# Kernel tuning notes

Hardware: AMD Instinct MI355X
Metric: run time of the kernel (lower is better)

The kernel has to match this reference:

```python
import jax, jax.numpy as jnp
import numpy as np

B, C, T = 1024, 64, 275
S = 10            # number of subjects
EMB = 184         # encoder embedding dim
PROJ = 1024       # projector dim
LN_EPS = 1e-5


def setup_inputs() -> dict:
    key = jax.random.key(0)
    ks = jax.random.split(key, 12)
    sc = lambda *shape: 1.0 / np.sqrt(shape[-1] if len(shape) > 1 else 1.0)
    return {
        "eeg": jax.random.normal(ks[0], (B, C, T), dtype=jnp.float32),
        "subject_ids": jax.random.randint(ks[1], (B,), 0, S, dtype=jnp.int64),
        # per-subject Linear(T, T): y = x @ W.T + b
        "subj_W": jax.random.normal(ks[2], (S, T, T), dtype=jnp.float32) / np.sqrt(T),
        "subj_b": jax.random.normal(ks[3], (S, T), dtype=jnp.float32) * 0.02,
        # encoder stub: flatten (C*T) -> Linear -> EMB
        "enc_W": jax.random.normal(ks[4], (C * T, EMB), dtype=jnp.float32) / np.sqrt(C * T),
        "enc_b": jnp.zeros((EMB,), dtype=jnp.float32),
        # projector: Linear(EMB, PROJ) -> ResidualAdd(GELU -> Linear(PROJ, PROJ)) -> LayerNorm
        "W1": jax.random.normal(ks[5], (EMB, PROJ), dtype=jnp.float32) / np.sqrt(EMB),
        "b1": jnp.zeros((PROJ,), dtype=jnp.float32),
        "W2": jax.random.normal(ks[6], (PROJ, PROJ), dtype=jnp.float32) / np.sqrt(PROJ),
        "b2": jnp.zeros((PROJ,), dtype=jnp.float32),
        "gamma": jnp.ones((PROJ,), dtype=jnp.float32),
        "beta": jnp.zeros((PROJ,), dtype=jnp.float32),
    }


def reference(eeg, subject_ids, subj_W, subj_b, enc_W, enc_b, W1, b1, W2, b2, gamma, beta):
    # --- subject-wise alignment: grouped gather -> linear -> scatter ---
    # Vectorized form of the per-subject loop: each row b uses weight subj_W[sid[b]].
    Wg = subj_W[subject_ids]              # [B, T, T]
    bg = subj_b[subject_ids]              # [B, T]
    # torch Linear: y = x @ W.T + b  ->  y[b,c,u] = sum_t eeg[b,c,t] * Wg[b,u,t]
    x = jnp.einsum("bct,but->bcu", eeg, Wg) + bg[:, None, :]   # [B, C, T]

    # --- encoder stub (SpatioTemporalCNN placeholder): flatten + linear ---
    h = x.reshape(x.shape[0], -1) @ enc_W + enc_b              # [B, EMB]

    # --- MLPProjector ---
    h = h @ W1 + b1                                            # [B, PROJ]
    r = jax.nn.gelu(h, approximate=False) @ W2 + b2            # dropout is identity at eval
    h = h + r
    # LayerNorm over last dim
    mu = jnp.mean(h, axis=-1, keepdims=True)
    var = jnp.mean(jnp.square(h - mu), axis=-1, keepdims=True)
    out = (h - mu) * jax.lax.rsqrt(var + LN_EPS) * gamma + beta
    return out
```

## Files before the change

kernel.cpp:

```cpp
#include <hip/hip_runtime.h>
#include <hip/hip_bf16.h>
#include <math.h>

#define B_N    1024
#define C_N    64
#define T_N    275
#define S_N    10
#define EMB_N  184
#define PROJ_N 1024
#define CT_N   (C_N * T_N)
#define TP     288
#define KP2    (C_N * TP)
#define EMBP   192
#define KZ2    16
#define KC2    (KP2 / KZ2)
#define KZ5    2
#define GMAX   264
#define ESTR   296

#define SEC_W   0
#define SEC_E   810
#define SEC_1   1002
#define SEC_2   1050
#define SEC_G   1306
#define SEC_N   1307

typedef unsigned short u16;
typedef __attribute__((ext_vector_type(8))) short short8;
typedef __attribute__((ext_vector_type(4))) short short4v;
typedef __attribute__((ext_vector_type(4))) float f32x4;

#define MFMA16(a,b,c) __builtin_amdgcn_mfma_f32_16x16x32_bf16(a, b, c, 0, 0, 0)

__device__ __forceinline__ u16 f2bf(float f) {
    __hip_bfloat16 h = __float2bfloat16(f);
    return *reinterpret_cast<u16*>(&h);
}
__device__ __forceinline__ float gelu_exact(float v) {
    return 0.5f * v * (1.0f + erff(v * 0.70710678118654752f));
}
__device__ __forceinline__ void gload16(const void* g, void* lds) {
    __builtin_amdgcn_global_load_lds(
        (const __attribute__((address_space(1))) void*)g,
        (__attribute__((address_space(3))) void*)lds, 16, 0, 0);
}

__global__ __launch_bounds__(256) void p_all(
    const int* __restrict__ sid, const float* __restrict__ W,
    const float* __restrict__ encW, const float* __restrict__ W1,
    const float* __restrict__ W2, const float* __restrict__ subj_b,
    u16* __restrict__ Wb, u16* __restrict__ eT, u16* __restrict__ w1t,
    u16* __restrict__ w2t, int* __restrict__ bsq, float* __restrict__ sbp)
{
    __shared__ char smem[16640];
    const int blk = blockIdx.x;
    const int tid = threadIdx.x;

    if (blk < SEC_E) {
        int idx4 = blk * 256 + tid;
        if (idx4 >= S_N * TP * TP / 4) return;
        int o = idx4 * 4;
        int row = o / TP, t = o - row * TP;
        int s = row / TP, u = row - s * TP;
        short4v pk;
        #pragma unroll
        for (int e = 0; e < 4; ++e) {
            float v = (u < T_N && t + e < T_N)
                ? W[((size_t)s * T_N + u) * T_N + t + e] : 0.f;
            pk[e] = (short)f2bf(v);
        }
        *reinterpret_cast<short4v*>(Wb + o) = pk;
        return;
    }
    if (blk < SEC_1) {
        float (*tile)[65] = (float(*)[65])smem;
        int local = blk - SEC_E;
        const int c = local / 3;
        const int n0 = (local % 3) * 64;
        for (int u0 = 0; u0 < TP; u0 += 64) {
            int wlen = (TP - u0 < 64) ? (TP - u0) : 64;
            __syncthreads();
            for (int l = tid; l < 4096; l += 256) {
                int i = l >> 6, j = l & 63;
                int u = u0 + i, n = n0 + j;
                float v = 0.f;
                if (u < T_N && n < EMB_N)
                    v = encW[((size_t)c * T_N + u) * EMB_N + n];
                tile[i][j] = v;
            }
            __syncthreads();
            for (int l = tid; l < 4096; l += 256) {
                int j = l >> 6, i = l & 63;
                if (i < wlen)
                    eT[(size_t)(n0 + j) * KP2 + (size_t)c * TP + u0 + i] =
                        f2bf(tile[i][j]);
            }
        }
        return;
    }
    if (blk < SEC_2) {
        float (*tile)[65] = (float(*)[65])smem;
        int local = blk - SEC_1;
        const int k0 = (local % 3) * 64, n0 = (local / 3) * 64;
        for (int l = tid; l < 4096; l += 256) {
            int i = l >> 6, j = l & 63;
            float v = (k0 + i < EMB_N) ? W1[(size_t)(k0 + i) * PROJ_N + n0 + j] : 0.f;
            tile[i][j] = v;
        }
        __syncthreads();
        for (int l = tid; l < 4096; l += 256) {
            int j = l >> 6, i = l & 63;
            w1t[(size_t)(n0 + j) * EMBP + k0 + i] = f2bf(tile[i][j]);
        }
        return;
    }
    if (blk < SEC_G) {
        float (*tile)[65] = (float(*)[65])smem;
        int local = blk - SEC_2;
        const int k0 = (local % 16) * 64, n0 = (local / 16) * 64;
        for (int l = tid; l < 4096; l += 256) {
            int i = l >> 6, j = l & 63;
            tile[i][j] = W2[(size_t)(k0 + i) * PROJ_N + n0 + j];
        }
        __syncthreads();
        for (int l = tid; l < 4096; l += 256) {
            int j = l >> 6, i = l & 63;
            w2t[(size_t)(n0 + j) * PROJ_N + k0 + i] = f2bf(tile[i][j]);
        }
        return;
    }
    {
        for (int i = tid; i < S_N * TP; i += 256) {
            int s = i / TP, u = i - s * TP;
            sbp[i] = (u < T_N) ? subj_b[s * T_N + u] : 0.f;
        }
        int* sgrp = (int*)smem;
        int* C    = (int*)(smem + 4096);
        int* tot  = (int*)(smem + 4096 + 640);
        for (int i = tid; i < 1024; i += 256) sgrp[i] = sid[i];
        for (int i = tid; i < 4 * GMAX; i += 256) bsq[i] = -1;
        __syncthreads();
        const int w4 = tid >> 6, lane = tid & 63;
        #pragma unroll
        for (int j = 0; j < 4; ++j) {
            int chunk = w4 * 4 + j;
            int sb = sgrp[chunk * 64 + lane];
            int myc = 0;
            for (int s = 0; s < S_N; ++s) {
                unsigned long long m = __ballot(sb == s);
                if (lane == s) myc = (int)__popcll(m);
            }
            if (lane < S_N) C[chunk * S_N + lane] = myc;
        }
        __syncthreads();
        if (tid < S_N) {
            int a = 0;
            for (int w2 = 0; w2 < 16; ++w2) a += C[w2 * S_N + tid];
            tot[tid] = a;
        }
        __syncthreads();
        #pragma unroll
        for (int rep = 0; rep < 4; ++rep) {
            int b = tid + rep * 256;
            int s = sgrp[b];
            int off = 0;
            for (int s2 = 0; s2 < S_N; ++s2)
                if (s2 < s) off += (tot[s2] + 3) & ~3;
            int chunk = b >> 6;
            int rank = 0;
            for (int w2 = 0; w2 < 16; ++w2)
                if (w2 < chunk) rank += C[w2 * S_N + s];
            for (int i = chunk * 64; i < b; ++i) rank += (sgrp[i] == s) ? 1 : 0;
            bsq[off + rank] = b;
        }
    }
}

__global__ __launch_bounds__(256) void k1v(
    const float* __restrict__ eeg, const int* __restrict__ sid,
    const u16* __restrict__ Wb, const float* __restrict__ sbp,
    const int* __restrict__ bsq, u16* __restrict__ xb)
{
    __shared__ __align__(16) u16 Es[64 * ESTR];
    __shared__ __align__(16) u16 Ws[2][TP * 32];
    const int g = blockIdx.x;
    const int b0 = bsq[g * 4];
    if (b0 < 0) return;
    const int p = blockIdx.y >> 1, ch = blockIdx.y & 1;
    const int s = sid[b0];
    const int tid = threadIdx.x;
    const int w = tid >> 6, lane = tid & 63;
    const int bi = w >> 1, uh = w & 1;
    const int lrow = lane & 15, lk = lane >> 4;
    const int b = bsq[g * 4 + p * 2 + bi];
    const u16* Wr = Wb + (size_t)s * TP * TP;

    #define K1_WSTAGE(st, ks)                                                  \
        for (int l = tid; l < TP * 4; l += 256) {                              \
            int u_ = l >> 2, q_ = l & 3;                                       \
            gload16(Wr + (size_t)u_ * TP + (ks) * 32 + ((q_ ^ ((u_ >> 1) & 3)) << 3), \
                    &Ws[st][l * 8]);                                           \
        }

    K1_WSTAGE(0, 0);
    #pragma unroll
    for (int reg = 0; reg < 2; ++reg) {
        int bstage = bsq[g * 4 + p * 2 + reg]; if (bstage < 0) bstage = b0;
        const float4* src4 = reinterpret_cast<const float4*>(
            eeg + (size_t)bstage * CT_N + ch * 32 * T_N);
        for (int l = tid; l < (32 * T_N) / 4; l += 256) {
            float4 v = src4[l];
            float vv[4] = { v.x, v.y, v.z, v.w };
            int o = l * 4;
            int r = o / T_N, c0 = o - r * T_N;
            #pragma unroll
            for (int e = 0; e < 4; ++e) {
                int r2 = r, c2 = c0 + e;
                if (c2 >= T_N) { r2++; c2 -= T_N; }
                Es[(reg * 32 + r2) * ESTR + c2] = f2bf(vv[e]);
            }
        }
    }
    for (int l = tid; l < 64 * (TP - T_N); l += 256) {
        int r = l / (TP - T_N), c = T_N + (l - r * (TP - T_N));
        Es[r * ESTR + c] = 0;
    }
    __syncthreads();

    f32x4 acc[9][2] = {};
    for (int ks = 0; ks < 9; ++ks) {
        const int st = ks & 1;
        if (ks < 8) K1_WSTAGE(st ^ 1, ks + 1);
        short8 ef[2];
        #pragma unroll
        for (int cf = 0; cf < 2; ++cf)
            ef[cf] = *reinterpret_cast<const short8*>(
                &Es[(bi * 32 + cf * 16 + lrow) * ESTR + ks * 32 + lk * 8]);
        #pragma unroll
        for (int uf = 0; uf < 9; ++uf) {
            int u = uh * 144 + uf * 16 + lrow;
            int chunk = u * 4 + (lk ^ ((u >> 1) & 3));
            short8 av = *reinterpret_cast<const short8*>(&Ws[st][chunk * 8]);
            acc[uf][0] = MFMA16(av, ef[0], acc[uf][0]);
            acc[uf][1] = MFMA16(av, ef[1], acc[uf][1]);
        }
        __syncthreads();
    }

    if (b < 0) return;
    u16* xrow = xb + (size_t)b * KP2 + (size_t)(ch * 32) * TP;
    #pragma unroll
    for (int uf = 0; uf < 9; ++uf) {
        int ub = uh * 144 + uf * 16 + 4 * lk;
        float4 b4 = *reinterpret_cast<const float4*>(sbp + s * TP + ub);
        float bias[4] = { b4.x, b4.y, b4.z, b4.w };
        #pragma unroll
        for (int cf = 0; cf < 2; ++cf) {
            int c = cf * 16 + lrow;
            short4v pk;
            #pragma unroll
            for (int r = 0; r < 4; ++r)
                pk[r] = (ub + r < T_N) ? (short)f2bf(acc[uf][cf][r] + bias[r])
                                       : (short)0;
            *reinterpret_cast<short4v*>(xrow + (size_t)c * TP + ub) = pk;
        }
    }
    #undef K1_WSTAGE
}

__global__ __launch_bounds__(256) void k2_mfma(
    const u16* __restrict__ xb, const u16* __restrict__ eT,
    float* __restrict__ part)
{
    __shared__ __align__(16) u16 Ab[2][64 * 64];
    const int m0 = blockIdx.x * 64;
    const int kz = blockIdx.y;
    const int kbase = kz * KC2;
    const int tid = threadIdx.x;
    const int w = tid >> 6, lane = tid & 63;
    const int lrow = lane & 15, lk = lane >> 4;

    #define K2_STAGE(st, step)                                                 \
        _Pragma("unroll")                                                      \
        for (int p = 0; p < 2; ++p) {                                          \
            int l = tid + p * 256;                                             \
            int r_ = l >> 3, q_ = l & 7;                                       \
            gload16(xb + (size_t)(m0 + r_) * KP2 + kbase + (step) * 64 +       \
                        ((q_ ^ (r_ & 7)) << 3),                                \
                    &Ab[st][l * 8]);                                           \
        }
    #define K2_BLOAD(step, dst)                                                \
        _Pragma("unroll")                                                      \
        for (int ct = 0; ct < 3; ++ct)                                         \
            _Pragma("unroll")                                                  \
            for (int ki = 0; ki < 2; ++ki)                                     \
                dst[ct][ki] = *reinterpret_cast<const short8*>(                \
                    eT + (size_t)(48 * w + 16 * ct + lrow) * KP2 + kbase +     \
                    (step) * 64 + ki * 32 + 8 * lk);

    f32x4 acc[4][3] = {};
    short8 bf[3][2], bn[3][2];

    K2_STAGE(0, 0);
    K2_BLOAD(0, bf);
    __syncthreads();

    for (int step = 0; step < 18; ++step) {
        const int st = step & 1;
        if (step < 17) {
            K2_STAGE(st ^ 1, step + 1);
            K2_BLOAD(step + 1, bn);
        }
        #pragma unroll
        for (int ki = 0; ki < 2; ++ki)
            #pragma unroll
            for (int rt = 0; rt < 4; ++rt) {
                int m = 16 * rt + lrow;
                int chunk = m * 8 + ((4 * ki + lk) ^ (m & 7));
                short8 af = *reinterpret_cast<const short8*>(&Ab[st][chunk * 8]);
                #pragma unroll
                for (int ct = 0; ct < 3; ++ct)
                    acc[rt][ct] = MFMA16(af, bf[ct][ki], acc[rt][ct]);
            }
        __syncthreads();
        #pragma unroll
        for (int ct = 0; ct < 3; ++ct)
            #pragma unroll
            for (int ki = 0; ki < 2; ++ki) bf[ct][ki] = bn[ct][ki];
    }

    #pragma unroll
    for (int rt = 0; rt < 4; ++rt)
        #pragma unroll
        for (int ct = 0; ct < 3; ++ct) {
            int n = 48 * w + 16 * ct + lrow;
            #pragma unroll
            for (int r = 0; r < 4; ++r) {
                int m = m0 + 16 * rt + 4 * lk + r;
                part[((size_t)kz * B_N + m) * EMBP + n] = acc[rt][ct][r];
            }
        }
    #undef K2_STAGE
    #undef K2_BLOAD
}

__global__ __launch_bounds__(256) void k3_reduce(
    const float* __restrict__ part, const float* __restrict__ enc_b,
    u16* __restrict__ hb)
{
    int idx = blockIdx.x * 256 + threadIdx.x;
    if (idx >= B_N * EMBP) return;
    int n = idx % EMBP;
    float s = 0.f;
    if (n < EMB_N) {
        s = enc_b[n];
        #pragma unroll
        for (int z = 0; z < KZ2; ++z)
            s += part[(size_t)z * B_N * EMBP + idx];
    }
    hb[idx] = f2bf(s);
}

__global__ __launch_bounds__(256) void k4_mfma(
    const u16* __restrict__ hb, const u16* __restrict__ w1t,
    const float* __restrict__ b1, float* __restrict__ h1, u16* __restrict__ g)
{
    __shared__ __align__(16) u16 Ab[64 * EMBP];
    __shared__ __align__(16) u16 Bb[64 * EMBP];
    const int m0 = blockIdx.x * 64, n0 = blockIdx.y * 64;
    const int tid = threadIdx.x;
    const int w = tid >> 6, lane = tid & 63;
    const int wr = w >> 1, wc = w & 1;
    const int lrow = lane & 15, lk = lane >> 4;

    #pragma unroll
    for (int i = 0; i < 6; ++i) {
        int L = tid + i * 256;
        int row = L / 24, qp = L % 24;
        int ql = qp ^ (row & 7);
        gload16(hb  + (size_t)(m0 + row) * EMBP + ql * 8, &Ab[(size_t)L * 8]);
        gload16(w1t + (size_t)(n0 + row) * EMBP + ql * 8, &Bb[(size_t)L * 8]);
    }
    __syncthreads();

    f32x4 acc[2][2] = {};
    #pragma unroll
    for (int ks = 0; ks < 6; ++ks) {
        #pragma unroll
        for (int rt = 0; rt < 2; ++rt) {
            int c = 32 * wr + 16 * rt + lrow;
            short8 af = *reinterpret_cast<const short8*>(
                &Ab[c * EMBP + (((4 * ks + lk) ^ (c & 7)) * 8)]);
            #pragma unroll
            for (int ct = 0; ct < 2; ++ct) {
                int nl = 32 * wc + 16 * ct + lrow;
                short8 bfv = *reinterpret_cast<const short8*>(
                    &Bb[nl * EMBP + (((4 * ks + lk) ^ (nl & 7)) * 8)]);
                acc[rt][ct] = MFMA16(af, bfv, acc[rt][ct]);
            }
        }
    }
    #pragma unroll
    for (int rt = 0; rt < 2; ++rt)
        #pragma unroll
        for (int ct = 0; ct < 2; ++ct) {
            int n = n0 + 32 * wc + 16 * ct + lrow;
            #pragma unroll
            for (int r = 0; r < 4; ++r) {
                int m = m0 + 32 * wr + 16 * rt + 4 * lk + r;
                float v = acc[rt][ct][r] + b1[n];
                size_t o = (size_t)m * PROJ_N + n;
                h1[o] = v;
                g[o] = f2bf(gelu_exact(v));
            }
        }
}

__global__ __launch_bounds__(256) void k5_mfma(
    const u16* __restrict__ g, const u16* __restrict__ w2t,
    float* __restrict__ part2)
{
    __shared__ __align__(16) u16 Ab[2][64 * 64];
    __shared__ __align__(16) u16 Bb[2][64 * 64];
    const int m0 = blockIdx.x * 64, n0 = blockIdx.y * 64;
    const int kz = blockIdx.z;
    const int kbase = kz * (PROJ_N / KZ5);
    const int tid = threadIdx.x;
    const int w = tid >> 6, lane = tid & 63;
    const int wr = w >> 1, wc = w & 1;
    const int lrow = lane & 15, lk = lane >> 4;

    const int r0 = tid >> 3, q0 = tid & 7;
    const int r1 = (tid + 256) >> 3;
    const u16* a0 = g + (size_t)(m0 + r0) * PROJ_N + (q0 ^ (r0 & 7)) * 8;
    const u16* a1 = g + (size_t)(m0 + r1) * PROJ_N + (q0 ^ (r1 & 7)) * 8;
    const u16* b0 = w2t + (size_t)(n0 + r0) * PROJ_N + (q0 ^ (r0 & 7)) * 8;
    const u16* b1p = w2t + (size_t)(n0 + r1) * PROJ_N + (q0 ^ (r1 & 7)) * 8;

    f32x4 acc[2][2] = {};
    int buf = 0;
    gload16(a0 + kbase, &Ab[0][(size_t)(w * 64) * 8]);
    gload16(a1 + kbase, &Ab[0][(size_t)(w * 64 + 256) * 8]);
    gload16(b0 + kbase, &Bb[0][(size_t)(w * 64) * 8]);
    gload16(b1p + kbase, &Bb[0][(size_t)(w * 64 + 256) * 8]);
    __syncthreads();

    for (int step = 0; step < 8; ++step) {
        if (step < 7) {
            int k0 = kbase + (step + 1) * 64;
            gload16(a0 + k0, &Ab[buf ^ 1][(size_t)(w * 64) * 8]);
            gload16(a1 + k0, &Ab[buf ^ 1][(size_t)(w * 64 + 256) * 8]);
            gload16(b0 + k0, &Bb[buf ^ 1][(size_t)(w * 64) * 8]);
            gload16(b1p + k0, &Bb[buf ^ 1][(size_t)(w * 64 + 256) * 8]);
        }
        #pragma unroll
        for (int ki = 0; ki < 2; ++ki) {
            #pragma unroll
            for (int rt = 0; rt < 2; ++rt) {
                int c = 32 * wr + 16 * rt + lrow;
                short8 af = *reinterpret_cast<const short8*>(
                    &Ab[buf][c * 64 + (((lk + 4 * ki) ^ (c & 7)) * 8)]);
                #pragma unroll
                for (int ct = 0; ct < 2; ++ct) {
                    int nl = 32 * wc + 16 * ct + lrow;
                    short8 bfv = *reinterpret_cast<const short8*>(
                        &Bb[buf][nl * 64 + (((lk + 4 * ki) ^ (nl & 7)) * 8)]);
                    acc[rt][ct] = MFMA16(af, bfv, acc[rt][ct]);
                }
            }
        }
        __syncthreads();
        buf ^= 1;
    }
    #pragma unroll
    for (int rt = 0; rt < 2; ++rt)
        #pragma unroll
        for (int ct = 0; ct < 2; ++ct) {
            int n = n0 + 32 * wc + 16 * ct + lrow;
            #pragma unroll
            for (int r = 0; r < 4; ++r) {
                int m = m0 + 32 * wr + 16 * rt + 4 * lk + r;
                part2[(size_t)kz * B_N * PROJ_N + (size_t)m * PROJ_N + n] = acc[rt][ct][r];
            }
        }
}

__global__ __launch_bounds__(256) void k5r_ln(
    const float* __restrict__ part2, const float* __restrict__ h1,
    const float* __restrict__ b2, const float* __restrict__ gamma,
    const float* __restrict__ beta, float* __restrict__ out)
{
    const int m = blockIdx.x;
    const int tid = threadIdx.x;
    const float4* h4 = reinterpret_cast<const float4*>(h1 + (size_t)m * PROJ_N);
    const float4* p0 = reinterpret_cast<const float4*>(part2 + (size_t)m * PROJ_N);
    const float4* p1 = reinterpret_cast<const float4*>(part2 + (size_t)(B_N + m) * PROJ_N);
    const float4* b4 = reinterpret_cast<const float4*>(b2);
    float4 va = h4[tid], vb = p0[tid], vc = p1[tid], vd = b4[tid];
    float v[4] = { va.x + vb.x + vc.x + vd.x, va.y + vb.y + vc.y + vd.y,
                   va.z + vb.z + vc.z + vd.z, va.w + vb.w + vc.w + vd.w };
    float s = 0.f, sq = 0.f;
    #pragma unroll
    for (int i = 0; i < 4; ++i) { s += v[i]; sq += v[i] * v[i]; }
    #pragma unroll
    for (int off = 32; off > 0; off >>= 1) {
        s  += __shfl_down(s, off);
        sq += __shfl_down(sq, off);
    }
    __shared__ float ss[4], ssq[4];
    int wid = tid >> 6, lane = tid & 63;
    if (lane == 0) { ss[wid] = s; ssq[wid] = sq; }
    __syncthreads();
    if (tid == 0) {
        float a = 0.f, bsum = 0.f;
        #pragma unroll
        for (int q = 0; q < 4; ++q) { a += ss[q]; bsum += ssq[q]; }
        ss[0] = a; ssq[0] = bsum;
    }
    __syncthreads();
    float mu  = ss[0] * (1.0f / PROJ_N);
    float var = ssq[0] * (1.0f / PROJ_N) - mu * mu;
    float rs  = rsqrtf(var + 1e-5f);
    const float4 g4 = reinterpret_cast<const float4*>(gamma)[tid];
    const float4 be4 = reinterpret_cast<const float4*>(beta)[tid];
    float gg[4] = { g4.x, g4.y, g4.z, g4.w };
    float bb[4] = { be4.x, be4.y, be4.z, be4.w };
    float4 o4;
    float* op = reinterpret_cast<float*>(&o4);
    #pragma unroll
    for (int i = 0; i < 4; ++i) op[i] = (v[i] - mu) * rs * gg[i] + bb[i];
    reinterpret_cast<float4*>(out + (size_t)m * PROJ_N)[tid] = o4;
}

extern "C" void kernel_launch(void* const* d_in, const int* in_sizes, int n_in,
                              void* d_out, int out_size, void* d_ws, size_t ws_size,
                              hipStream_t stream)
{
    const float* eeg    = (const float*)d_in[0];
    const int*   sid    = (const int*)  d_in[1];
    const float* subj_W = (const float*)d_in[2];
    const float* subj_b = (const float*)d_in[3];
    const float* enc_W  = (const float*)d_in[4];
    const float* enc_b  = (const float*)d_in[5];
    const float* W1     = (const float*)d_in[6];
    const float* b1     = (const float*)d_in[7];
    const float* W2     = (const float*)d_in[8];
    const float* b2     = (const float*)d_in[9];
    const float* gamma  = (const float*)d_in[10];
    const float* beta   = (const float*)d_in[11];
    float* out = (float*)d_out;

    char* w = (char*)d_ws;
    u16*   xb    = (u16*)(w);
    u16*   Wb    = (u16*)(w + 37748736);
    u16*   eT    = (u16*)(w + 39407616);
    u16*   w1t   = (u16*)(w + 46485504);
    u16*   w2t   = (u16*)(w + 46878720);
    u16*   hb    = (u16*)(w + 48975872);
    float* h1    = (float*)(w + 49369088);
    u16*   g     = (u16*)(w + 53563392);
    float* sbp   = (float*)(w + 55660544);
    int*   bsq   = (int*)(w + 55672064);
    float* part  = (float*)(w + 55676288);
    float* part2 = (float*)(w + 68259200);

    p_all<<<dim3(SEC_N), 256, 0, stream>>>(sid, subj_W, enc_W, W1, W2, subj_b,
                                           Wb, eT, w1t, w2t, bsq, sbp);
    k1v  <<<dim3(GMAX, 4), 256, 0, stream>>>(eeg, sid, Wb, sbp, bsq, xb);
    k2_mfma<<<dim3(16, KZ2), 256, 0, stream>>>(xb, eT, part);
    k3_reduce<<<dim3((B_N * EMBP + 255) / 256), 256, 0, stream>>>(part, enc_b, hb);
    k4_mfma<<<dim3(16, 16), 256, 0, stream>>>(hb, w1t, b1, h1, g);
    k5_mfma<<<dim3(16, 16, KZ5), 256, 0, stream>>>(g, w2t, part2);
    k5r_ln <<<dim3(B_N), 256, 0, stream>>>(part2, h1, b2, gamma, beta, out);
}
```

Baseline: 130.9 us.

## Pre-convert EEG to padded bf16 and stream it via async LDS loads in k1

The prep kernel gains 1024 extra blocks that convert each EEG sample to a zero-padded bf16 layout with row stride 288. The subject-linear kernel becomes a 512-thread block handling four samples per subject group. It double-buffers both the weight tile and the swizzled EEG tile through global_load_lds each k-step, replacing the up-front fp32 load, convert and LDS scatter. It also raises wave priority around the MFMA loop. The trade is an extra global write and read of the bf16 EEG copy, which reuses the partials scratch region, and larger blocks that may lower occupancy.

```diff
diff --git a/kernel.cpp b/kernel.cpp
--- a/kernel.cpp
+++ b/kernel.cpp
@@ -16,14 +16,14 @@
 #define KC2    (KP2 / KZ2)
 #define KZ5    2
 #define GMAX   264
-#define ESTR   296
-
-#define SEC_W   0
-#define SEC_E   810
-#define SEC_1   1002
-#define SEC_2   1050
-#define SEC_G   1306
-#define SEC_N   1307
+
+#define SEC_EEG 0
+#define SEC_W   1024
+#define SEC_E   1834
+#define SEC_1   2026
+#define SEC_2   2074
+#define SEC_G   2330
+#define SEC_N   2331
 
 typedef unsigned short u16;
 typedef __attribute__((ext_vector_type(8))) short short8;
@@ -46,18 +46,40 @@
 }
 
 __global__ __launch_bounds__(256) void p_all(
-    const int* __restrict__ sid, const float* __restrict__ W,
-    const float* __restrict__ encW, const float* __restrict__ W1,
-    const float* __restrict__ W2, const float* __restrict__ subj_b,
-    u16* __restrict__ Wb, u16* __restrict__ eT, u16* __restrict__ w1t,
-    u16* __restrict__ w2t, int* __restrict__ bsq, float* __restrict__ sbp)
+    const float* __restrict__ eeg, const int* __restrict__ sid,
+    const float* __restrict__ W, const float* __restrict__ encW,
+    const float* __restrict__ W1, const float* __restrict__ W2,
+    const float* __restrict__ subj_b,
+    u16* __restrict__ eegb, u16* __restrict__ Wb, u16* __restrict__ eT,
+    u16* __restrict__ w1t, u16* __restrict__ w2t, int* __restrict__ bsq,
+    float* __restrict__ sbp)
 {
     __shared__ char smem[16640];
     const int blk = blockIdx.x;
     const int tid = threadIdx.x;
 
+    if (blk < SEC_W) {
+        const int b = blk;
+        const float* src = eeg + (size_t)b * CT_N;
+        u16* dst = eegb + (size_t)b * (C_N * TP);
+        #pragma unroll
+        for (int p = 0; p < 9; ++p) {
+            int L = tid + p * 256;
+            int r = L / 36, q8 = L - r * 36;
+            int t0 = q8 * 8;
+            short8 pk;
+            #pragma unroll
+            for (int e = 0; e < 8; ++e) {
+                int t = t0 + e;
+                float v = (t < T_N) ? src[r * T_N + t] : 0.f;
+                pk[e] = (short)f2bf(v);
+            }
+            *reinterpret_cast<short8*>(dst + r * TP + t0) = pk;
+        }
+        return;
+    }
     if (blk < SEC_E) {
-        int idx4 = blk * 256 + tid;
+        int idx4 = (blk - SEC_W) * 256 + tid;
         if (idx4 >= S_N * TP * TP / 4) return;
         int o = idx4 * 4;
         int row = o / TP, t = o - row * TP;
@@ -176,66 +198,60 @@
     }
 }
 
-__global__ __launch_bounds__(256) void k1v(
-    const float* __restrict__ eeg, const int* __restrict__ sid,
+__global__ __launch_bounds__(512) void k1x(
+    const u16* __restrict__ eegb, const int* __restrict__ sid,
     const u16* __restrict__ Wb, const float* __restrict__ sbp,
     const int* __restrict__ bsq, u16* __restrict__ xb)
 {
-    __shared__ __align__(16) u16 Es[64 * ESTR];
     __shared__ __align__(16) u16 Ws[2][TP * 32];
+    __shared__ __align__(16) u16 Es[2][128 * 32];
     const int g = blockIdx.x;
     const int b0 = bsq[g * 4];
     if (b0 < 0) return;
-    const int p = blockIdx.y >> 1, ch = blockIdx.y & 1;
+    const int ch = blockIdx.y;
     const int s = sid[b0];
     const int tid = threadIdx.x;
     const int w = tid >> 6, lane = tid & 63;
     const int bi = w >> 1, uh = w & 1;
     const int lrow = lane & 15, lk = lane >> 4;
-    const int b = bsq[g * 4 + p * 2 + bi];
+    const int b = bsq[g * 4 + bi];
     const u16* Wr = Wb + (size_t)s * TP * TP;
 
+    const int ar = tid >> 2, aq = tid & 3;
+    int bsa = bsq[g * 4 + (ar >> 5)]; if (bsa < 0) bsa = b0;
+    const u16* asrc = eegb + (size_t)bsa * (C_N * TP)
+                    + (size_t)(ch * 32 + (ar & 31)) * TP
+                    + ((aq ^ ((ar >> 1) & 3)) << 3);
+
     #define K1_WSTAGE(st, ks)                                                  \
-        for (int l = tid; l < TP * 4; l += 256) {                              \
+        for (int l = tid; l < TP * 4; l += 512) {                              \
             int u_ = l >> 2, q_ = l & 3;                                       \
             gload16(Wr + (size_t)u_ * TP + (ks) * 32 + ((q_ ^ ((u_ >> 1) & 3)) << 3), \
                     &Ws[st][l * 8]);                                           \
         }
+    #define K1_ASTAGE(st, ks)                                                  \
+        gload16(asrc + (ks) * 32, &Es[st][tid * 8]);
+
+    f32x4 acc[9][2] = {};
 
     K1_WSTAGE(0, 0);
-    #pragma unroll
-    for (int reg = 0; reg < 2; ++reg) {
-        int bstage = bsq[g * 4 + p * 2 + reg]; if (bstage < 0) bstage = b0;
-        const float4* src4 = reinterpret_cast<const float4*>(
-            eeg + (size_t)bstage * CT_N + ch * 32 * T_N);
-        for (int l = tid; l < (32 * T_N) / 4; l += 256) {
-            float4 v = src4[l];
-            float vv[4] = { v.x, v.y, v.z, v.w };
-            int o = l * 4;
-            int r = o / T_N, c0 = o - r * T_N;
-            #pragma unroll
-            for (int e = 0; e < 4; ++e) {
-                int r2 = r, c2 = c0 + e;
-                if (c2 >= T_N) { r2++; c2 -= T_N; }
-                Es[(reg * 32 + r2) * ESTR + c2] = f2bf(vv[e]);
-            }
-        }
-    }
-    for (int l = tid; l < 64 * (TP - T_N); l += 256) {
-        int r = l / (TP - T_N), c = T_N + (l - r * (TP - T_N));
-        Es[r * ESTR + c] = 0;
-    }
+    K1_ASTAGE(0, 0);
     __syncthreads();
 
-    f32x4 acc[9][2] = {};
     for (int ks = 0; ks < 9; ++ks) {
         const int st = ks & 1;
-        if (ks < 8) K1_WSTAGE(st ^ 1, ks + 1);
+        if (ks < 8) {
+            K1_WSTAGE(st ^ 1, ks + 1);
+            K1_ASTAGE(st ^ 1, ks + 1);
+        }
         short8 ef[2];
         #pragma unroll
-        for (int cf = 0; cf < 2; ++cf)
+        for (int cf = 0; cf < 2; ++cf) {
+            int rr = bi * 32 + cf * 16 + lrow;
             ef[cf] = *reinterpret_cast<const short8*>(
-                &Es[(bi * 32 + cf * 16 + lrow) * ESTR + ks * 32 + lk * 8]);
+                &Es[st][(rr * 4 + (lk ^ ((rr >> 1) & 3))) * 8]);
+        }
+        __builtin_amdgcn_s_setprio(1);
         #pragma unroll
         for (int uf = 0; uf < 9; ++uf) {
             int u = uh * 144 + uf * 16 + lrow;
@@ -244,6 +260,7 @@
             acc[uf][0] = MFMA16(av, ef[0], acc[uf][0]);
             acc[uf][1] = MFMA16(av, ef[1], acc[uf][1]);
         }
+        __builtin_amdgcn_s_setprio(0);
         __syncthreads();
     }
 
@@ -266,6 +283,7 @@
         }
     }
     #undef K1_WSTAGE
+    #undef K1_ASTAGE
 }
 
 __global__ __launch_bounds__(256) void k2_mfma(
@@ -561,12 +579,15 @@
     u16*   g     = (u16*)(w + 53563392);
     float* sbp   = (float*)(w + 55660544);
     int*   bsq   = (int*)(w + 55672064);
-    float* part  = (float*)(w + 55676288);
-    float* part2 = (float*)(w + 68259200);
-
-    p_all<<<dim3(SEC_N), 256, 0, stream>>>(sid, subj_W, enc_W, W1, W2, subj_b,
-                                           Wb, eT, w1t, w2t, bsq, sbp);
-    k1v  <<<dim3(GMAX, 4), 256, 0, stream>>>(eeg, sid, Wb, sbp, bsq, xb);
+    char*  scr   = w + 55676288;
+    u16*   eegb  = (u16*)scr;
+    float* part  = (float*)scr;
+    float* part2 = (float*)(scr + 12582912);
+
+    p_all<<<dim3(SEC_N), 256, 0, stream>>>(eeg, sid, subj_W, enc_W, W1, W2,
+                                           subj_b, eegb, Wb, eT, w1t, w2t,
+                                           bsq, sbp);
+    k1x  <<<dim3(GMAX, 2), 512, 0, stream>>>(eegb, sid, Wb, sbp, bsq, xb);
     k2_mfma<<<dim3(16, KZ2), 256, 0, stream>>>(xb, eT, part);
     k3_reduce<<<dim3((B_N * EMBP + 255) / 256), 256, 0, stream>>>(part, enc_b, hb);
     k4_mfma<<<dim3(16, 16), 256, 0, stream>>>(hb, w1t, b1, h1, g);
```

Result: faster. 125.7 us (-4.0%).

## Restructure subject-alignment kernel into 512-thread blocks with pipelined async EEG loads

Applied to the files above, without the earlier changes.

Replaces k1v with k1y, which runs 8 waves per block and covers all four batch rows of a group. Each staged subject-weight tile is therefore reused across twice as many rows, halving the block count and the weight staging traffic. Instead of converting the whole EEG slab to bf16 in LDS before the loop, each k-step now async-loads a swizzled fp32 chunk with 4-byte global_load_lds, double-buffered alongside the weight tiles, and converts to bf16 when building fragments. It also raises wave priority around the MFMA block. The cost is more LDS instructions and conversions per step. The padded tail columns load column-0 data, which stays correct only because the padded weights are zero.

```diff
diff --git a/kernel.cpp b/kernel.cpp
--- a/kernel.cpp
+++ b/kernel.cpp
@@ -16,7 +16,6 @@
 #define KC2    (KP2 / KZ2)
 #define KZ5    2
 #define GMAX   264
-#define ESTR   296
 
 #define SEC_W   0
 #define SEC_E   810
@@ -43,6 +42,11 @@
     __builtin_amdgcn_global_load_lds(
         (const __attribute__((address_space(1))) void*)g,
         (__attribute__((address_space(3))) void*)lds, 16, 0, 0);
+}
+__device__ __forceinline__ void gload4(const void* g, void* lds) {
+    __builtin_amdgcn_global_load_lds(
+        (const __attribute__((address_space(1))) void*)g,
+        (__attribute__((address_space(3))) void*)lds, 4, 0, 0);
 }
 
 __global__ __launch_bounds__(256) void p_all(
@@ -176,66 +180,89 @@
     }
 }
 
-__global__ __launch_bounds__(256) void k1v(
+__global__ __launch_bounds__(512) void k1y(
     const float* __restrict__ eeg, const int* __restrict__ sid,
     const u16* __restrict__ Wb, const float* __restrict__ sbp,
     const int* __restrict__ bsq, u16* __restrict__ xb)
 {
-    __shared__ __align__(16) u16 Es[64 * ESTR];
-    __shared__ __align__(16) u16 Ws[2][TP * 32];
+    __shared__ __align__(16) u16   Ws[2][TP * 32];
+    __shared__ __align__(16) float Ea[2][128 * 32];
     const int g = blockIdx.x;
     const int b0 = bsq[g * 4];
     if (b0 < 0) return;
-    const int p = blockIdx.y >> 1, ch = blockIdx.y & 1;
+    const int ch = blockIdx.y;
     const int s = sid[b0];
     const int tid = threadIdx.x;
     const int w = tid >> 6, lane = tid & 63;
     const int bi = w >> 1, uh = w & 1;
     const int lrow = lane & 15, lk = lane >> 4;
-    const int b = bsq[g * 4 + p * 2 + bi];
+    const int b = bsq[g * 4 + bi];
     const u16* Wr = Wb + (size_t)s * TP * TP;
 
+    const int ep  = tid & 31;
+    const int re  = tid >> 5;
+    const int sel = (((ep >> 2) ^ (re & 7)) << 2) + (ep & 3);
+    const int sel8 = (256 + sel < T_N) ? (256 + sel) : 0;
+    const float* eb0; const float* eb1; const float* eb2; const float* eb3;
+    {
+        int b00 = bsq[g*4+0]; if (b00 < 0) b00 = b0;
+        int b01 = bsq[g*4+1]; if (b01 < 0) b01 = b0;
+        int b02 = bsq[g*4+2]; if (b02 < 0) b02 = b0;
+        int b03 = bsq[g*4+3]; if (b03 < 0) b03 = b0;
+        const float* base = eeg + (size_t)(ch * 32 + re) * T_N;
+        eb0 = base + (size_t)b00 * CT_N;
+        eb1 = base + (size_t)b01 * CT_N;
+        eb2 = base + (size_t)b02 * CT_N;
+        eb3 = base + (size_t)b03 * CT_N;
+    }
+
     #define K1_WSTAGE(st, ks)                                                  \
-        for (int l = tid; l < TP * 4; l += 256) {                              \
+        for (int l = tid; l < TP * 4; l += 512) {                              \
             int u_ = l >> 2, q_ = l & 3;                                       \
             gload16(Wr + (size_t)u_ * TP + (ks) * 32 + ((q_ ^ ((u_ >> 1) & 3)) << 3), \
                     &Ws[st][l * 8]);                                           \
         }
+    #define K1_ASTAGE(st, tofs)                                                \
+        {   gload4(eb0 + 0 * T_N + (tofs), &Ea[st][tid + 0 * 512]);            \
+            gload4(eb0 + 16 * T_N + (tofs), &Ea[st][tid + 1 * 512]);           \
+            gload4(eb1 + 0 * T_N + (tofs), &Ea[st][tid + 2 * 512]);            \
+            gload4(eb1 + 16 * T_N + (tofs), &Ea[st][tid + 3 * 512]);           \
+            gload4(eb2 + 0 * T_N + (tofs), &Ea[st][tid + 4 * 512]);            \
+            gload4(eb2 + 16 * T_N + (tofs), &Ea[st][tid + 5 * 512]);           \
+            gload4(eb3 + 0 * T_N + (tofs), &Ea[st][tid + 6 * 512]);            \
+            gload4(eb3 + 16 * T_N + (tofs), &Ea[st][tid + 7 * 512]);           \
+        }
+
+    f32x4 acc[9][2] = {};
 
     K1_WSTAGE(0, 0);
-    #pragma unroll
-    for (int reg = 0; reg < 2; ++reg) {
-        int bstage = bsq[g * 4 + p * 2 + reg]; if (bstage < 0) bstage = b0;
-        const float4* src4 = reinterpret_cast<const float4*>(
-            eeg + (size_t)bstage * CT_N + ch * 32 * T_N);
-        for (int l = tid; l < (32 * T_N) / 4; l += 256) {
-            float4 v = src4[l];
-            float vv[4] = { v.x, v.y, v.z, v.w };
-            int o = l * 4;
-            int r = o / T_N, c0 = o - r * T_N;
-            #pragma unroll
-            for (int e = 0; e < 4; ++e) {
-                int r2 = r, c2 = c0 + e;
-                if (c2 >= T_N) { r2++; c2 -= T_N; }
-                Es[(reg * 32 + r2) * ESTR + c2] = f2bf(vv[e]);
-            }
-        }
-    }
-    for (int l = tid; l < 64 * (TP - T_N); l += 256) {
-        int r = l / (TP - T_N), c = T_N + (l - r * (TP - T_N));
-        Es[r * ESTR + c] = 0;
-    }
+    K1_ASTAGE(0, sel);
     __syncthreads();
 
-    f32x4 acc[9][2] = {};
     for (int ks = 0; ks < 9; ++ks) {
         const int st = ks & 1;
-        if (ks < 8) K1_WSTAGE(st ^ 1, ks + 1);
+        if (ks < 8) {
+            K1_WSTAGE(st ^ 1, ks + 1);
+            const int tofs = (ks + 1 < 8) ? ((ks + 1) * 32 + sel) : sel8;
+            K1_ASTAGE(st ^ 1, tofs);
+        }
         short8 ef[2];
         #pragma unroll
-        for (int cf = 0; cf < 2; ++cf)
-            ef[cf] = *reinterpret_cast<const short8*>(
-                &Es[(bi * 32 + cf * 16 + lrow) * ESTR + ks * 32 + lk * 8]);
+        for (int cf = 0; cf < 2; ++cf) {
+            int rr = bi * 32 + cf * 16 + lrow;
+            int r7 = rr & 7;
+            float4 f0 = *reinterpret_cast<const float4*>(
+                &Ea[st][rr * 32 + (((2 * lk) ^ r7) << 2)]);
+            float4 f1 = *reinterpret_cast<const float4*>(
+                &Ea[st][rr * 32 + (((2 * lk + 1) ^ r7) << 2)]);
+            short8 pk;
+            pk[0] = (short)f2bf(f0.x); pk[1] = (short)f2bf(f0.y);
+            pk[2] = (short)f2bf(f0.z); pk[3] = (short)f2bf(f0.w);
+            pk[4] = (short)f2bf(f1.x); pk[5] = (short)f2bf(f1.y);
+            pk[6] = (short)f2bf(f1.z); pk[7] = (short)f2bf(f1.w);
+            ef[cf] = pk;
+        }
+        __builtin_amdgcn_s_setprio(1);
         #pragma unroll
         for (int uf = 0; uf < 9; ++uf) {
             int u = uh * 144 + uf * 16 + lrow;
@@ -244,6 +271,7 @@
             acc[uf][0] = MFMA16(av, ef[0], acc[uf][0]);
             acc[uf][1] = MFMA16(av, ef[1], acc[uf][1]);
         }
+        __builtin_amdgcn_s_setprio(0);
         __syncthreads();
     }
 
@@ -266,6 +294,7 @@
         }
     }
     #undef K1_WSTAGE
+    #undef K1_ASTAGE
 }
 
 __global__ __launch_bounds__(256) void k2_mfma(
@@ -566,7 +595,7 @@
 
     p_all<<<dim3(SEC_N), 256, 0, stream>>>(sid, subj_W, enc_W, W1, W2, subj_b,
                                            Wb, eT, w1t, w2t, bsq, sbp);
-    k1v  <<<dim3(GMAX, 4), 256, 0, stream>>>(eeg, sid, Wb, sbp, bsq, xb);
+    k1y  <<<dim3(GMAX, 2), 512, 0, stream>>>(eeg, sid, Wb, sbp, bsq, xb);
     k2_mfma<<<dim3(16, KZ2), 256, 0, stream>>>(xb, eT, part);
     k3_reduce<<<dim3((B_N * EMBP + 255) / 256), 256, 0, stream>>>(part, enc_b, hb);
     k4_mfma<<<dim3(16, 16), 256, 0, stream>>>(hb, w1t, b1, h1, g);
```

Result: faster. 127.0 us (-3.0%).
